# Kernel optimization log

Measured on AMD Instinct MI355X. Metric: run time of the kernel, lower is better.

Reference implementation:

```python
import jax, jax.numpy as jnp
import numpy as np

B, N, DIN, DOUT = 8, 2048, 512, 512
EDGE_P = 0.01  # edge probability for the random binary adjacency


def setup_inputs() -> dict:
    key = jax.random.key(0)
    k1, k2, k3, k4 = jax.random.split(key, 4)
    inputs = jax.random.normal(k1, (B, N, DIN), dtype=jnp.float32)
    # binary dense adjacency (dense_to_sparse discards weights -> edges are adj != 0)
    adj = (jax.random.uniform(k2, (B, N, N)) < EDGE_P).astype(jnp.float32)
    W = jax.random.normal(k3, (DIN, DOUT), dtype=jnp.float32) / np.sqrt(DIN)
    b = jax.random.normal(k4, (DOUT,), dtype=jnp.float32) * 0.01
    return {"inputs": inputs, "adj": adj, "W": W, "b": b}


def _gcn_norm(adj):
    # binary edge mask (edge weights from dense_to_sparse are discarded)
    A = (adj != 0).astype(adj.dtype)
    # add remaining self-loops: force diagonal to 1
    eye = jnp.eye(A.shape[-1], dtype=A.dtype)
    A = jnp.maximum(A, eye)
    deg = A.sum(axis=-1)                       # [B, N]
    dinv = jnp.where(deg > 0, jax.lax.rsqrt(deg), 0.0)
    # D^-1/2 (A + I) D^-1/2
    return dinv[..., :, None] * A * dinv[..., None, :]


def reference(inputs, adj, W, b):
    norm = _gcn_norm(adj)                      # [B, N, N]
    h = jnp.einsum('bnf,fo->bno', inputs, W)   # linear (no internal bias)
    agg = jnp.einsum('bnm,bmo->bno', norm, h)  # degree-normalized aggregation
    return jnp.tanh(agg + b)
```

## Files before the change

### kernel.cpp

```cpp
#include <hip/hip_runtime.h>
#include <hip/hip_bf16.h>
#include <math.h>


#define NROWS 16384
#define NCOLS 2048
#define DF    512
#define CAP   64

typedef __attribute__((ext_vector_type(8))) short bf16x8;
typedef __attribute__((ext_vector_type(4))) float f32x4;

typedef const void __attribute__((address_space(1))) gvoid_t;
typedef void __attribute__((address_space(3))) svoid_t;

__global__ __launch_bounds__(256) void wt_kernel(
    const float* __restrict__ W, __hip_bfloat16* __restrict__ WT) {
  __shared__ float t[64][65];
  const int b2 = blockIdx.x;
  const int bx = b2 & 7, by = b2 >> 3;
  const int tid = threadIdx.x;
  const int tx = tid & 63, ty = tid >> 6;
  #pragma unroll
  for (int i = 0; i < 16; ++i)
    t[ty + i * 4][tx] = W[(size_t)(by * 64 + ty + i * 4) * DF + bx * 64 + tx];
  __syncthreads();
  #pragma unroll
  for (int i = 0; i < 16; ++i)
    WT[(size_t)(bx * 64 + ty + i * 4) * DF + by * 64 + tx] =
        __float2bfloat16(t[tx][ty + i * 4]);
}

__global__ __launch_bounds__(256) void fused_k1(
    const float* __restrict__ X, const __hip_bfloat16* __restrict__ WT,
    const float* __restrict__ adj, __hip_bfloat16* __restrict__ H,
    int* __restrict__ cnt, int* __restrict__ edges, float* __restrict__ dinv) {
  __shared__ __hip_bfloat16 As[128 * 32];
  __shared__ __hip_bfloat16 Bs[128 * 32];
  const int id = blockIdx.x;
  const int tid = threadIdx.x;
  const int lane = tid & 63;
  const int w = tid >> 6;

  if (id < 512) {
    const int xcd = id & 7;
    const int jj = id >> 3;
    const int p  = xcd * 16 + (jj >> 2);
    const int bm = p * 128;
    const int bn = (jj & 3) * 128;

    const int wm = (w >> 1) * 64;
    const int wn = (w & 1) * 64;
    const int srow = tid >> 2;
    const int scol = (tid & 3) * 8;
    const int arow = tid >> 1;
    const int akh  = (tid & 1) * 16;
    const int kl = (lane >> 4) * 8;
    const int rl = lane & 15;

    f32x4 acc[4][4] = {};

    for (int k0 = 0; k0 < DF; k0 += 32) {
      #pragma unroll
      for (int i = 0; i < 2; ++i) {
        const __hip_bfloat16* gb = WT + (size_t)(bn + i * 64 + srow) * DF + k0 + scol;
        char* lb = (char*)Bs + i * 4096 + w * 1024;
        __builtin_amdgcn_global_load_lds((gvoid_t*)gb, (svoid_t*)lb, 16, 0, 0);
      }
      const float* gaf = X + (size_t)(bm + arow) * DF + k0 + akh;
      float xs[16];
      *(float4*)&xs[0]  = ((const float4*)gaf)[0];
      *(float4*)&xs[4]  = ((const float4*)gaf)[1];
      *(float4*)&xs[8]  = ((const float4*)gaf)[2];
      *(float4*)&xs[12] = ((const float4*)gaf)[3];
      union { __hip_bfloat16 h[16]; uint4 q[2]; } pk;
      #pragma unroll
      for (int i = 0; i < 16; ++i) pk.h[i] = __float2bfloat16(xs[i]);
      char* la = (char*)As + arow * 64 + akh * 2;
      ((uint4*)la)[0] = pk.q[0];
      ((uint4*)la)[1] = pk.q[1];

      __syncthreads();

      bf16x8 af[4], bf[4];
      #pragma unroll
      for (int mi = 0; mi < 4; ++mi)
        af[mi] = *(const bf16x8*)&As[(wm + mi * 16 + rl) * 32 + kl];
      #pragma unroll
      for (int ni = 0; ni < 4; ++ni)
        bf[ni] = *(const bf16x8*)&Bs[(wn + ni * 16 + rl) * 32 + kl];
      #pragma unroll
      for (int mi = 0; mi < 4; ++mi)
        #pragma unroll
        for (int ni = 0; ni < 4; ++ni)
          acc[mi][ni] = __builtin_amdgcn_mfma_f32_16x16x32_bf16(af[mi], bf[ni], acc[mi][ni], 0, 0, 0);
      __syncthreads();
    }

    const int rq = (lane >> 4) * 4;
    #pragma unroll
    for (int mi = 0; mi < 4; ++mi)
      #pragma unroll
      for (int ni = 0; ni < 4; ++ni) {
        const int col = bn + wn + ni * 16 + rl;
        #pragma unroll
        for (int j = 0; j < 4; ++j) {
          const int row = bm + wm + mi * 16 + rq + j;
          H[(size_t)row * DF + col] = __float2bfloat16(acc[mi][ni][j]);
        }
      }
  } else {
    const int r = (id - 512) * 4 + w;
    const int n = r & (NCOLS - 1);
    const float4* row4 = (const float4*)(adj + (size_t)r * NCOLS);
    const unsigned long long lt = (1ull << lane) - 1ull;
    int base = 0;
    #pragma unroll
    for (int k = 0; k < NCOLS / 256; ++k) {
      const float4 v = row4[k * 64 + lane];
      const int c0 = k * 256 + lane * 4;
      const bool f0 = (v.x != 0.0f) || (c0 + 0 == n);
      const bool f1 = (v.y != 0.0f) || (c0 + 1 == n);
      const bool f2 = (v.z != 0.0f) || (c0 + 2 == n);
      const bool f3 = (v.w != 0.0f) || (c0 + 3 == n);
      const unsigned long long m0 = __ballot(f0);
      const unsigned long long m1 = __ballot(f1);
      const unsigned long long m2 = __ballot(f2);
      const unsigned long long m3 = __ballot(f3);
      const int n0 = __popcll(m0), n1 = __popcll(m1), n2 = __popcll(m2), n3 = __popcll(m3);
      if (f0) { int p = base + __popcll(m0 & lt);                if (p < CAP) edges[(size_t)r * CAP + p] = c0 + 0; }
      if (f1) { int p = base + n0 + __popcll(m1 & lt);           if (p < CAP) edges[(size_t)r * CAP + p] = c0 + 1; }
      if (f2) { int p = base + n0 + n1 + __popcll(m2 & lt);      if (p < CAP) edges[(size_t)r * CAP + p] = c0 + 2; }
      if (f3) { int p = base + n0 + n1 + n2 + __popcll(m3 & lt); if (p < CAP) edges[(size_t)r * CAP + p] = c0 + 3; }
      base += n0 + n1 + n2 + n3;
    }
    if (lane == 0) {
      cnt[r] = base < CAP ? base : CAP;
      dinv[r] = rsqrtf((float)base);
    }
  }
}

__global__ __launch_bounds__(256) void aggregate(
    const __hip_bfloat16* __restrict__ h, const int* __restrict__ cnt,
    const int* __restrict__ edges, const float* __restrict__ dinv,
    const float* __restrict__ bias, float* __restrict__ out) {
  const int lane = threadIdx.x & 63;
  const int wv = threadIdx.x >> 6;
  const int j = blockIdx.x * 4 + wv;
  const int r = (j & 7) * NCOLS + (j >> 3);
  const int b = r >> 11;
  const int c = cnt[r];
  int   ml = 0;
  float wl = 0.0f;
  if (lane < c) {
    ml = edges[(size_t)r * CAP + lane];
    wl = dinv[(b << 11) + ml];
  }
  const float4* b4 = (const float4*)bias;
  const float4 bb0 = b4[lane * 2];
  const float4 bb1 = b4[lane * 2 + 1];

  float acc[8] = {0.f, 0.f, 0.f, 0.f, 0.f, 0.f, 0.f, 0.f};
  const uint4* hbase = (const uint4*)(h + ((size_t)(b << 11)) * DF);
  for (int e = 0; e < c; ++e) {
    const int   m  = __shfl(ml, e);
    const float wt = __shfl(wl, e);
    const uint4 hv = hbase[(size_t)m * 64 + lane];
    acc[0] += wt * __uint_as_float(hv.x << 16);
    acc[1] += wt * __uint_as_float(hv.x & 0xffff0000u);
    acc[2] += wt * __uint_as_float(hv.y << 16);
    acc[3] += wt * __uint_as_float(hv.y & 0xffff0000u);
    acc[4] += wt * __uint_as_float(hv.z << 16);
    acc[5] += wt * __uint_as_float(hv.z & 0xffff0000u);
    acc[6] += wt * __uint_as_float(hv.w << 16);
    acc[7] += wt * __uint_as_float(hv.w & 0xffff0000u);
  }
  const float dn = dinv[r];
  float4 o0, o1;
  o0.x = tanhf(acc[0] * dn + bb0.x);
  o0.y = tanhf(acc[1] * dn + bb0.y);
  o0.z = tanhf(acc[2] * dn + bb0.z);
  o0.w = tanhf(acc[3] * dn + bb0.w);
  o1.x = tanhf(acc[4] * dn + bb1.x);
  o1.y = tanhf(acc[5] * dn + bb1.y);
  o1.z = tanhf(acc[6] * dn + bb1.z);
  o1.w = tanhf(acc[7] * dn + bb1.w);
  float4* op = (float4*)(out + (size_t)r * DF + lane * 8);
  op[0] = o0;
  op[1] = o1;
}

extern "C" void kernel_launch(void* const* d_in, const int* in_sizes, int n_in,
                              void* d_out, int out_size, void* d_ws, size_t ws_size,
                              hipStream_t stream) {
  const float* X    = (const float*)d_in[0];
  const float* adj  = (const float*)d_in[1];
  const float* W    = (const float*)d_in[2];
  const float* bias = (const float*)d_in[3];
  float* out = (float*)d_out;

  char* ws = (char*)d_ws;
  __hip_bfloat16* h    = (__hip_bfloat16*)(ws);
  __hip_bfloat16* WT   = (__hip_bfloat16*)(ws + 16777216);
  float*          dinv = (float*)(ws + 17301504);
  int*            cnt  = (int*)  (ws + 17367040);
  int*            edges= (int*)  (ws + 17432576);

  wt_kernel<<<64, 256, 0, stream>>>(W, WT);
  fused_k1<<<512 + NROWS / 4, 256, 0, stream>>>(X, WT, adj, h, cnt, edges, dinv);
  aggregate<<<NROWS / 4, 256, 0, stream>>>(h, cnt, edges, dinv, bias, out);
}
```

Before: 87.78 us.

## Move adjacency scan into transpose prep kernel and double-buffer GEMM LDS

The adjacency edge-list scan moves out of the fused GEMM kernel and into the W transpose kernel, so the GEMM becomes a standalone 512-block launch. The GEMM now double-buffers its A and B LDS tiles and prefetches the next k-slice while the MFMAs run, which removes one barrier per iteration. The scan also loads all eight float4 values of each row up front to raise memory-level parallelism. In exchange, the scan no longer overlaps with GEMM compute in the same launch, and the GEMM uses twice the LDS.

```diff
diff --git a/kernel.cpp b/kernel.cpp
--- a/kernel.cpp
+++ b/kernel.cpp
@@ -14,131 +14,151 @@
 typedef const void __attribute__((address_space(1))) gvoid_t;
 typedef void __attribute__((address_space(3))) svoid_t;
 
-__global__ __launch_bounds__(256) void wt_kernel(
-    const float* __restrict__ W, __hip_bfloat16* __restrict__ WT) {
+__global__ __launch_bounds__(256) void prep(
+    const float* __restrict__ W, __hip_bfloat16* __restrict__ WT,
+    const float* __restrict__ adj, int* __restrict__ cnt,
+    int* __restrict__ edges, float* __restrict__ dinv) {
   __shared__ float t[64][65];
-  const int b2 = blockIdx.x;
-  const int bx = b2 & 7, by = b2 >> 3;
+  const int id = blockIdx.x;
   const int tid = threadIdx.x;
-  const int tx = tid & 63, ty = tid >> 6;
+  if (id < 64) {
+    const int bx = id & 7, by = id >> 3;
+    const int tx = tid & 63, ty = tid >> 6;
+    #pragma unroll
+    for (int i = 0; i < 16; ++i)
+      t[ty + i * 4][tx] = W[(size_t)(by * 64 + ty + i * 4) * DF + bx * 64 + tx];
+    __syncthreads();
+    #pragma unroll
+    for (int i = 0; i < 16; ++i)
+      WT[(size_t)(bx * 64 + ty + i * 4) * DF + by * 64 + tx] =
+          __float2bfloat16(t[tx][ty + i * 4]);
+    return;
+  }
+  const int lane = tid & 63;
+  const int wv = tid >> 6;
+  const int r = (id - 64) * 4 + wv;
+  const int n = r & (NCOLS - 1);
+  const float4* row4 = (const float4*)(adj + (size_t)r * NCOLS);
+  float4 v[8];
   #pragma unroll
-  for (int i = 0; i < 16; ++i)
-    t[ty + i * 4][tx] = W[(size_t)(by * 64 + ty + i * 4) * DF + bx * 64 + tx];
-  __syncthreads();
+  for (int k = 0; k < 8; ++k) v[k] = row4[k * 64 + lane];
+  const unsigned long long lt = (1ull << lane) - 1ull;
+  int base = 0;
   #pragma unroll
-  for (int i = 0; i < 16; ++i)
-    WT[(size_t)(bx * 64 + ty + i * 4) * DF + by * 64 + tx] =
-        __float2bfloat16(t[tx][ty + i * 4]);
-}
-
-__global__ __launch_bounds__(256) void fused_k1(
+  for (int k = 0; k < 8; ++k) {
+    const int c0 = k * 256 + lane * 4;
+    const bool f0 = (v[k].x != 0.0f) || (c0 + 0 == n);
+    const bool f1 = (v[k].y != 0.0f) || (c0 + 1 == n);
+    const bool f2 = (v[k].z != 0.0f) || (c0 + 2 == n);
+    const bool f3 = (v[k].w != 0.0f) || (c0 + 3 == n);
+    const unsigned long long m0 = __ballot(f0);
+    const unsigned long long m1 = __ballot(f1);
+    const unsigned long long m2 = __ballot(f2);
+    const unsigned long long m3 = __ballot(f3);
+    const int n0 = __popcll(m0), n1 = __popcll(m1), n2 = __popcll(m2), n3 = __popcll(m3);
+    if (f0) { int p = base + __popcll(m0 & lt);                if (p < CAP) edges[(size_t)r * CAP + p] = c0 + 0; }
+    if (f1) { int p = base + n0 + __popcll(m1 & lt);           if (p < CAP) edges[(size_t)r * CAP + p] = c0 + 1; }
+    if (f2) { int p = base + n0 + n1 + __popcll(m2 & lt);      if (p < CAP) edges[(size_t)r * CAP + p] = c0 + 2; }
+    if (f3) { int p = base + n0 + n1 + n2 + __popcll(m3 & lt); if (p < CAP) edges[(size_t)r * CAP + p] = c0 + 3; }
+    base += n0 + n1 + n2 + n3;
+  }
+  if (lane == 0) {
+    cnt[r] = base < CAP ? base : CAP;
+    dinv[r] = rsqrtf((float)base);
+  }
+}
+
+__global__ __launch_bounds__(256) void gemm_k(
     const float* __restrict__ X, const __hip_bfloat16* __restrict__ WT,
-    const float* __restrict__ adj, __hip_bfloat16* __restrict__ H,
-    int* __restrict__ cnt, int* __restrict__ edges, float* __restrict__ dinv) {
-  __shared__ __hip_bfloat16 As[128 * 32];
-  __shared__ __hip_bfloat16 Bs[128 * 32];
-  const int id = blockIdx.x;
+    __hip_bfloat16* __restrict__ H) {
+  __shared__ __hip_bfloat16 As[2][128 * 32];
+  __shared__ __hip_bfloat16 Bs[2][128 * 32];
   const int tid = threadIdx.x;
   const int lane = tid & 63;
   const int w = tid >> 6;
-
-  if (id < 512) {
-    const int xcd = id & 7;
-    const int jj = id >> 3;
-    const int p  = xcd * 16 + (jj >> 2);
-    const int bm = p * 128;
-    const int bn = (jj & 3) * 128;
-
-    const int wm = (w >> 1) * 64;
-    const int wn = (w & 1) * 64;
-    const int srow = tid >> 2;
-    const int scol = (tid & 3) * 8;
-    const int arow = tid >> 1;
-    const int akh  = (tid & 1) * 16;
-    const int kl = (lane >> 4) * 8;
-    const int rl = lane & 15;
-
-    f32x4 acc[4][4] = {};
-
-    for (int k0 = 0; k0 < DF; k0 += 32) {
-      #pragma unroll
-      for (int i = 0; i < 2; ++i) {
-        const __hip_bfloat16* gb = WT + (size_t)(bn + i * 64 + srow) * DF + k0 + scol;
-        char* lb = (char*)Bs + i * 4096 + w * 1024;
-        __builtin_amdgcn_global_load_lds((gvoid_t*)gb, (svoid_t*)lb, 16, 0, 0);
-      }
-      const float* gaf = X + (size_t)(bm + arow) * DF + k0 + akh;
-      float xs[16];
-      *(float4*)&xs[0]  = ((const float4*)gaf)[0];
-      *(float4*)&xs[4]  = ((const float4*)gaf)[1];
-      *(float4*)&xs[8]  = ((const float4*)gaf)[2];
-      *(float4*)&xs[12] = ((const float4*)gaf)[3];
-      union { __hip_bfloat16 h[16]; uint4 q[2]; } pk;
-      #pragma unroll
-      for (int i = 0; i < 16; ++i) pk.h[i] = __float2bfloat16(xs[i]);
-      char* la = (char*)As + arow * 64 + akh * 2;
-      ((uint4*)la)[0] = pk.q[0];
-      ((uint4*)la)[1] = pk.q[1];
-
-      __syncthreads();
-
-      bf16x8 af[4], bf[4];
-      #pragma unroll
-      for (int mi = 0; mi < 4; ++mi)
-        af[mi] = *(const bf16x8*)&As[(wm + mi * 16 + rl) * 32 + kl];
+  const int id = blockIdx.x;
+  const int xcd = id & 7;
+  const int jj = id >> 3;
+  const int bm = (xcd * 16 + (jj >> 2)) * 128;
+  const int bn = (jj & 3) * 128;
+
+  const int wm = (w >> 1) * 64;
+  const int wn = (w & 1) * 64;
+  const int srow = tid >> 2;
+  const int scol = (tid & 3) * 8;
+  const int arow = tid >> 1;
+  const int akh  = (tid & 1) * 16;
+  const int kl = (lane >> 4) * 8;
+  const int rl = lane & 15;
+
+  f32x4 acc[4][4] = {};
+  float4 ar0, ar1, ar2, ar3;
+
+  #define LOAD_A(k0)  do {                                              \
+    const float4* g = (const float4*)(X + (size_t)(bm + arow) * DF + (k0) + akh); \
+    ar0 = g[0]; ar1 = g[1]; ar2 = g[2]; ar3 = g[3]; } while (0)
+
+  #define STAGE_B(k0, buf)  do {                                        \
+    _Pragma("unroll")                                                   \
+    for (int i = 0; i < 2; ++i) {                                       \
+      const __hip_bfloat16* gb = WT + (size_t)(bn + i * 64 + srow) * DF + (k0) + scol; \
+      char* lb = (char*)&Bs[buf][0] + i * 4096 + w * 1024;              \
+      __builtin_amdgcn_global_load_lds((gvoid_t*)gb, (svoid_t*)lb, 16, 0, 0); \
+    } } while (0)
+
+  #define WRITE_A(buf)  do {                                            \
+    float xs[16];                                                       \
+    *(float4*)&xs[0] = ar0; *(float4*)&xs[4] = ar1;                     \
+    *(float4*)&xs[8] = ar2; *(float4*)&xs[12] = ar3;                    \
+    union { __hip_bfloat16 h[16]; uint4 q[2]; } pk;                     \
+    _Pragma("unroll")                                                   \
+    for (int i = 0; i < 16; ++i) pk.h[i] = __float2bfloat16(xs[i]);     \
+    char* la = (char*)&As[buf][0] + arow * 64 + akh * 2;                \
+    ((uint4*)la)[0] = pk.q[0];                                          \
+    ((uint4*)la)[1] = pk.q[1]; } while (0)
+
+  LOAD_A(0);
+  STAGE_B(0, 0);
+  WRITE_A(0);
+  __syncthreads();
+
+  for (int t = 0; t < 16; ++t) {
+    const int cur = t & 1, nxt = cur ^ 1;
+    if (t < 15) {
+      LOAD_A((t + 1) * 32);
+      STAGE_B((t + 1) * 32, nxt);
+    }
+    bf16x8 af[4], bf[4];
+    #pragma unroll
+    for (int mi = 0; mi < 4; ++mi)
+      af[mi] = *(const bf16x8*)&As[cur][(wm + mi * 16 + rl) * 32 + kl];
+    #pragma unroll
+    for (int ni = 0; ni < 4; ++ni)
+      bf[ni] = *(const bf16x8*)&Bs[cur][(wn + ni * 16 + rl) * 32 + kl];
+    #pragma unroll
+    for (int mi = 0; mi < 4; ++mi)
       #pragma unroll
       for (int ni = 0; ni < 4; ++ni)
-        bf[ni] = *(const bf16x8*)&Bs[(wn + ni * 16 + rl) * 32 + kl];
+        acc[mi][ni] = __builtin_amdgcn_mfma_f32_16x16x32_bf16(af[mi], bf[ni], acc[mi][ni], 0, 0, 0);
+    if (t < 15) WRITE_A(nxt);
+    __syncthreads();
+  }
+
+  const int rq = (lane >> 4) * 4;
+  #pragma unroll
+  for (int mi = 0; mi < 4; ++mi)
+    #pragma unroll
+    for (int ni = 0; ni < 4; ++ni) {
+      const int col = bn + wn + ni * 16 + rl;
       #pragma unroll
-      for (int mi = 0; mi < 4; ++mi)
-        #pragma unroll
-        for (int ni = 0; ni < 4; ++ni)
-          acc[mi][ni] = __builtin_amdgcn_mfma_f32_16x16x32_bf16(af[mi], bf[ni], acc[mi][ni], 0, 0, 0);
-      __syncthreads();
+      for (int j = 0; j < 4; ++j) {
+        const int row = bm + wm + mi * 16 + rq + j;
+        H[(size_t)row * DF + col] = __float2bfloat16(acc[mi][ni][j]);
+      }
     }
-
-    const int rq = (lane >> 4) * 4;
-    #pragma unroll
-    for (int mi = 0; mi < 4; ++mi)
-      #pragma unroll
-      for (int ni = 0; ni < 4; ++ni) {
-        const int col = bn + wn + ni * 16 + rl;
-        #pragma unroll
-        for (int j = 0; j < 4; ++j) {
-          const int row = bm + wm + mi * 16 + rq + j;
-          H[(size_t)row * DF + col] = __float2bfloat16(acc[mi][ni][j]);
-        }
-      }
-  } else {
-    const int r = (id - 512) * 4 + w;
-    const int n = r & (NCOLS - 1);
-    const float4* row4 = (const float4*)(adj + (size_t)r * NCOLS);
-    const unsigned long long lt = (1ull << lane) - 1ull;
-    int base = 0;
-    #pragma unroll
-    for (int k = 0; k < NCOLS / 256; ++k) {
-      const float4 v = row4[k * 64 + lane];
-      const int c0 = k * 256 + lane * 4;
-      const bool f0 = (v.x != 0.0f) || (c0 + 0 == n);
-      const bool f1 = (v.y != 0.0f) || (c0 + 1 == n);
-      const bool f2 = (v.z != 0.0f) || (c0 + 2 == n);
-      const bool f3 = (v.w != 0.0f) || (c0 + 3 == n);
-      const unsigned long long m0 = __ballot(f0);
-      const unsigned long long m1 = __ballot(f1);
-      const unsigned long long m2 = __ballot(f2);
-      const unsigned long long m3 = __ballot(f3);
-      const int n0 = __popcll(m0), n1 = __popcll(m1), n2 = __popcll(m2), n3 = __popcll(m3);
-      if (f0) { int p = base + __popcll(m0 & lt);                if (p < CAP) edges[(size_t)r * CAP + p] = c0 + 0; }
-      if (f1) { int p = base + n0 + __popcll(m1 & lt);           if (p < CAP) edges[(size_t)r * CAP + p] = c0 + 1; }
-      if (f2) { int p = base + n0 + n1 + __popcll(m2 & lt);      if (p < CAP) edges[(size_t)r * CAP + p] = c0 + 2; }
-      if (f3) { int p = base + n0 + n1 + n2 + __popcll(m3 & lt); if (p < CAP) edges[(size_t)r * CAP + p] = c0 + 3; }
-      base += n0 + n1 + n2 + n3;
-    }
-    if (lane == 0) {
-      cnt[r] = base < CAP ? base : CAP;
-      dinv[r] = rsqrtf((float)base);
-    }
-  }
+  #undef LOAD_A
+  #undef STAGE_B
+  #undef WRITE_A
 }
 
 __global__ __launch_bounds__(256) void aggregate(
@@ -207,7 +227,7 @@
   int*            cnt  = (int*)  (ws + 17367040);
   int*            edges= (int*)  (ws + 17432576);
 
-  wt_kernel<<<64, 256, 0, stream>>>(W, WT);
-  fused_k1<<<512 + NROWS / 4, 256, 0, stream>>>(X, WT, adj, h, cnt, edges, dinv);
+  prep<<<64 + NROWS / 4, 256, 0, stream>>>(W, WT, adj, cnt, edges, dinv);
+  gemm_k<<<512, 256, 0, stream>>>(X, WT, h);
   aggregate<<<NROWS / 4, 256, 0, stream>>>(h, cnt, edges, dinv, bias, out);
 }
```

After: 83.04 us. 5.4% less time.
